# Kernel optimization log

Hardware: AMD Instinct MI355X
Metric: run time of the kernel (lower is better)

The kernel has to match this reference:

```python
import jax, jax.numpy as jnp
import numpy as np

B = 262144
NUM_FEA = 256          # input feature dim, split into two towers of 128
HIDDEN = [64, 32, 16]  # tower hidden units
CO_FEA = 32            # 2 * HIDDEN[-1], features entering co-attention
EMB = 8                # per-feature embedding dim
OUT_DIM = 16           # final Dense(16)


def setup_inputs() -> dict:
    key = jax.random.key(0)
    ks = jax.random.split(key, 12)
    mid = NUM_FEA // 2
    def glorot(k, shape):
        fan_in, fan_out = shape[0], shape[1]
        lim = np.sqrt(6.0 / (fan_in + fan_out)).astype(np.float32)
        return jax.random.uniform(k, shape, jnp.float32, -lim, lim)
    return {
        "x": jax.random.normal(ks[0], (B, NUM_FEA), jnp.float32),
        # shared tower (weight_share=True -> only mod_dnn1 is used)
        "W1": glorot(ks[1], (mid, HIDDEN[0])), "b1": jnp.zeros((HIDDEN[0],), jnp.float32),
        "W2": glorot(ks[2], (HIDDEN[0], HIDDEN[1])), "b2": jnp.zeros((HIDDEN[1],), jnp.float32),
        "W3": glorot(ks[3], (HIDDEN[1], HIDDEN[2])), "b3": jnp.zeros((HIDDEN[2],), jnp.float32),
        # 32 per-feature Dense(8) layers on scalar inputs, stacked: weight [32,8], bias [32,8]
        "W_emb": glorot(ks[4], (CO_FEA, EMB)),
        "b_emb": jnp.zeros((CO_FEA, EMB), jnp.float32),
        # bilinear co-attention matrix
        "M": glorot(ks[5], (EMB, EMB)),
        # final Dense(16, relu) for mix='concat'
        "W_out": glorot(ks[6], (CO_FEA, OUT_DIM)),
        "b_out": jnp.zeros((OUT_DIM,), jnp.float32),
    }


def reference(x, W1, b1, W2, b2, W3, b3, W_emb, b_emb, M, W_out, b_out):
    mid = x.shape[1] // 2

    def tower(h):
        h = jax.nn.relu(h @ W1 + b1)
        h = jax.nn.relu(h @ W2 + b2)
        h = jax.nn.relu(h @ W3 + b3)
        return h

    left = tower(x[:, :mid])      # [B,16]
    right = tower(x[:, mid:])     # [B,16] (weight_share=True)
    out = jnp.concatenate([left, right], axis=-1)  # [B,32]

    # 32 tiny Dense(emb) on scalar features, batched: [B,32,1]*[32,8] + [32,8]
    emb = out[:, :, None] * W_emb[None, :, :] + b_emb[None, :, :]  # [B,32,8]
    cmid = out.shape[1] // 2  # 16
    l, r = emb[:, :cmid, :], emb[:, cmid:, :]

    G = jnp.tanh(jnp.einsum('bie,ef,bjf->bij', l, M, r))  # [B,16,16]
    lr = jax.nn.softmax(G.sum(axis=1), axis=-1)           # [B,16]
    rl = jax.nn.softmax(G.sum(axis=2), axis=-1)           # [B,16]
    a = jnp.concatenate([lr, rl], axis=-1)                # [B,32]

    out = out * a
    # mix == 'concat' -> Dense(16, relu)
    return jax.nn.relu(out @ W_out + b_out)               # [B,16]
```

## Files before the change

### kernel.cpp

```cpp
#include <hip/hip_runtime.h>

typedef __attribute__((ext_vector_type(8))) short bf16x8;
typedef __attribute__((ext_vector_type(4))) float f32x4;

#define MFMA16(a, b, c) __builtin_amdgcn_mfma_f32_16x16x32_bf16(a, b, c, 0, 0, 0)

__device__ __forceinline__ unsigned short f2bf(float f) {
    unsigned u = __builtin_bit_cast(unsigned, f);
    u += 0x7FFFu + ((u >> 16) & 1u);
    return (unsigned short)(u >> 16);
}
__device__ __forceinline__ float bf2f(unsigned short h) {
    return __builtin_bit_cast(float, (unsigned)h << 16);
}

__device__ __forceinline__ void split8(const float* v, bf16x8& hi, bf16x8& lo) {
    unsigned* hp = reinterpret_cast<unsigned*>(&hi);
    unsigned* lp = reinterpret_cast<unsigned*>(&lo);
    #pragma unroll
    for (int q = 0; q < 4; ++q) {
        const float a = v[2 * q], b = v[2 * q + 1];
        unsigned hpair;
        asm("v_cvt_pk_bf16_f32 %0, %1, %2" : "=v"(hpair) : "v"(a), "v"(b));
        const float ha = __builtin_bit_cast(float, hpair << 16);
        const float hb = __builtin_bit_cast(float, hpair & 0xFFFF0000u);
        const float ra = a - ha, rb = b - hb;
        unsigned lpair;
        asm("v_cvt_pk_bf16_f32 %0, %1, %2" : "=v"(lpair) : "v"(ra), "v"(rb));
        hp[q] = hpair;
        lp[q] = lpair;
    }
}

__global__ void prep_kernel(const float* __restrict__ W1,
                            const float* __restrict__ W2,
                            const float* __restrict__ W3,
                            const float* __restrict__ W_emb,
                            const float* __restrict__ b_emb,
                            const float* __restrict__ M,
                            float* __restrict__ pqrs,
                            unsigned short* __restrict__ w1h,
                            unsigned short* __restrict__ w1l,
                            unsigned short* __restrict__ wsm) {
    const int t = threadIdx.x;
    const float C2 = 2.8853900817779268f;
    {
        const int j = t >> 4;
        const int i = t & 15;
        float mr[8], mb[8];
        #pragma unroll
        for (int e = 0; e < 8; ++e) {
            float ar = 0.f, ab = 0.f;
            #pragma unroll
            for (int f = 0; f < 8; ++f) {
                const float m = M[e * 8 + f];
                ar = fmaf(m, W_emb[(16 + j) * 8 + f], ar);
                ab = fmaf(m, b_emb[(16 + j) * 8 + f], ab);
            }
            mr[e] = ar; mb[e] = ab;
        }
        float P = 0.f, Q = 0.f, R = 0.f, S = 0.f;
        #pragma unroll
        for (int e = 0; e < 8; ++e) {
            const float lw = W_emb[i * 8 + e];
            const float lb = b_emb[i * 8 + e];
            P = fmaf(lw, mr[e], P);
            Q = fmaf(lw, mb[e], Q);
            R = fmaf(lb, mr[e], R);
            S = fmaf(lb, mb[e], S);
        }
        pqrs[0 * 256 + j * 16 + i] = C2 * P;
        pqrs[1 * 256 + j * 16 + i] = C2 * Q;
        pqrs[2 * 256 + j * 16 + i] = C2 * R;
        pqrs[3 * 256 + j * 16 + i] = C2 * S;
    }
    for (int e = 0; e < 32; ++e) {
        const int idx = t * 32 + e;
        const int i = idx & 7, lane = (idx >> 3) & 63;
        const int n = (idx >> 9) & 3, kt = idx >> 11;
        const int k = kt * 32 + (lane >> 4) * 8 + i;
        const int c = n * 16 + (lane & 15);
        const float v = W1[k * 64 + c];
        const unsigned short h = f2bf(v);
        w1h[idx] = h;
        w1l[idx] = f2bf(v - bf2f(h));
    }
    for (int e = 0; e < 8; ++e) {
        const int idx = t * 8 + e;
        const int i = idx & 7, lane = (idx >> 3) & 63;
        const int n = (idx >> 9) & 1, kt = (idx >> 10) & 1;
        const int k = kt * 32 + (lane >> 4) * 8 + i;
        const int c = n * 16 + (lane & 15);
        const float v = W2[k * 32 + c];
        const unsigned short h = f2bf(v);
        wsm[idx] = h;
        wsm[2048 + idx] = f2bf(v - bf2f(h));
    }
    for (int e = 0; e < 2; ++e) {
        const int idx = t * 2 + e;
        const int i = idx & 7, lane = (idx >> 3) & 63;
        const int k = (lane >> 4) * 8 + i;
        const int c = lane & 15;
        const float v = W3[k * 16 + c];
        const unsigned short h = f2bf(v);
        wsm[4096 + idx] = h;
        wsm[4608 + idx] = f2bf(v - bf2f(h));
    }
}

__global__ __launch_bounds__(256, 3) void fused_kernel(
    const float* __restrict__ x,
    const unsigned short* __restrict__ w1h,
    const unsigned short* __restrict__ w1l,
    const unsigned short* __restrict__ wsm,
    const float* __restrict__ b1, const float* __restrict__ b2,
    const float* __restrict__ b3,
    const float* __restrict__ pqrs,
    const float* __restrict__ W_out, const float* __restrict__ b_out,
    float* __restrict__ y) {
    __shared__ float s_tr[4][16 * 68];
    __shared__ float s_h3[4][16 * 130];

    const int tid = threadIdx.x;
    const int l  = tid & 63;
    const int wv = tid >> 6;
    const int lm = l & 15;
    const int lg = l >> 4;

    const unsigned short* w2h = wsm;
    const unsigned short* w2l = wsm + 2048;
    const unsigned short* w3h = wsm + 4096;
    const unsigned short* w3l = wsm + 4608;

    float b1v[4], b2v[2];
    #pragma unroll
    for (int n = 0; n < 4; ++n) b1v[n] = b1[n * 16 + lm];
    #pragma unroll
    for (int n = 0; n < 2; ++n) b2v[n] = b2[n * 16 + lm];
    const float b3v = b3[lm];

    const long tr0 = (long)blockIdx.x * 512 + wv * 128;
    float* tb  = s_tr[wv];
    float* h3b = s_h3[wv];

    float4 xb[2][8];
    {
        const float* xp = x + (tr0 + lm) * 128 + lg * 8;
        #pragma unroll
        for (int kt = 0; kt < 4; ++kt) {
            xb[0][2 * kt]     = *(const float4*)(xp + kt * 32);
            xb[0][2 * kt + 1] = *(const float4*)(xp + kt * 32 + 4);
        }
    }

    #pragma unroll
    for (int tile = 0; tile < 8; ++tile) {
        const int cur = tile & 1, nxt = cur ^ 1;
        if (tile < 7) {
            const float* xp = x + (tr0 + (tile + 1) * 16 + lm) * 128 + lg * 8;
            #pragma unroll
            for (int kt = 0; kt < 4; ++kt) {
                xb[nxt][2 * kt]     = *(const float4*)(xp + kt * 32);
                xb[nxt][2 * kt + 1] = *(const float4*)(xp + kt * 32 + 4);
            }
        }
        f32x4 acc[4];
        #pragma unroll
        for (int n = 0; n < 4; ++n) acc[n] = f32x4{b1v[n], b1v[n], b1v[n], b1v[n]};
        #pragma unroll
        for (int kt = 0; kt < 4; ++kt) {
            const float4 a = xb[cur][2 * kt], b = xb[cur][2 * kt + 1];
            const float xv[8] = {a.x, a.y, a.z, a.w, b.x, b.y, b.z, b.w};
            bf16x8 xh, xl; split8(xv, xh, xl);
            #pragma unroll
            for (int n = 0; n < 4; ++n) {
                const int fo = ((kt * 4 + n) * 64 + l) * 8;
                const bf16x8 wh = *(const bf16x8*)(w1h + fo);
                const bf16x8 wl = *(const bf16x8*)(w1l + fo);
                acc[n] = MFMA16(xh, wh, acc[n]);
                acc[n] = MFMA16(xl, wh, acc[n]);
                acc[n] = MFMA16(xh, wl, acc[n]);
            }
        }
        #pragma unroll
        for (int n = 0; n < 4; ++n)
            #pragma unroll
            for (int r = 0; r < 4; ++r)
                tb[(lg * 4 + r) * 68 + n * 16 + lm] = fmaxf(acc[n][r], 0.f);
        f32x4 acc2[2];
        #pragma unroll
        for (int n = 0; n < 2; ++n) acc2[n] = f32x4{b2v[n], b2v[n], b2v[n], b2v[n]};
        #pragma unroll
        for (int kt = 0; kt < 2; ++kt) {
            const float* ap = tb + lm * 68 + kt * 32 + lg * 8;
            const float4 h0 = *(const float4*)(ap);
            const float4 h1 = *(const float4*)(ap + 4);
            const float hv[8] = {h0.x, h0.y, h0.z, h0.w, h1.x, h1.y, h1.z, h1.w};
            bf16x8 hh, hl; split8(hv, hh, hl);
            #pragma unroll
            for (int n = 0; n < 2; ++n) {
                const int fo = ((kt * 2 + n) * 64 + l) * 8;
                const bf16x8 wh = *(const bf16x8*)(w2h + fo);
                const bf16x8 wl = *(const bf16x8*)(w2l + fo);
                acc2[n] = MFMA16(hh, wh, acc2[n]);
                acc2[n] = MFMA16(hl, wh, acc2[n]);
                acc2[n] = MFMA16(hh, wl, acc2[n]);
            }
        }
        #pragma unroll
        for (int n = 0; n < 2; ++n)
            #pragma unroll
            for (int r = 0; r < 4; ++r)
                tb[(lg * 4 + r) * 68 + n * 16 + lm] = fmaxf(acc2[n][r], 0.f);
        f32x4 acc3 = f32x4{b3v, b3v, b3v, b3v};
        {
            const float* ap = tb + lm * 68 + lg * 8;
            const float4 h0 = *(const float4*)(ap);
            const float4 h1 = *(const float4*)(ap + 4);
            const float hv[8] = {h0.x, h0.y, h0.z, h0.w, h1.x, h1.y, h1.z, h1.w};
            bf16x8 hh, hl; split8(hv, hh, hl);
            const bf16x8 wh = *(const bf16x8*)(w3h + l * 8);
            const bf16x8 wl = *(const bf16x8*)(w3l + l * 8);
            acc3 = MFMA16(hh, wh, acc3);
            acc3 = MFMA16(hl, wh, acc3);
            acc3 = MFMA16(hh, wl, acc3);
        }
        #pragma unroll
        for (int r = 0; r < 4; ++r)
            h3b[lm * 130 + tile * 16 + lg * 4 + r] = fmaxf(acc3[r], 0.f);
    }

    float oL[16], oR[16];
    #pragma unroll
    for (int c = 0; c < 16; ++c) {
        const float2 v = *(const float2*)(h3b + c * 130 + 2 * l);
        oL[c] = v.x;
        oR[c] = v.y;
    }

    float sir[16];
    #pragma unroll
    for (int i = 0; i < 16; ++i) sir[i] = 0.f;
    float sjv[16];
    #pragma unroll
    for (int j = 0; j < 16; ++j) {
        const float r = oR[j];
        const float* __restrict__ Pr = pqrs +       j * 16;
        const float* __restrict__ Qr = pqrs + 256 + j * 16;
        const float* __restrict__ Rr = pqrs + 512 + j * 16;
        const float* __restrict__ Sr = pqrs + 768 + j * 16;
        float accr = 0.f;
        #pragma unroll
        for (int i = 0; i < 16; ++i) {
            const float t1 = fmaf(r, Pr[i], Qr[i]);
            const float t2 = fmaf(r, Rr[i], Sr[i]);
            const float z  = fmaf(oL[i], t1, t2);
            const float e  = __builtin_amdgcn_exp2f(z);
            const float rc = __builtin_amdgcn_rcpf(e + 1.0f);
            accr   += rc;
            sir[i] += rc;
        }
        sjv[j] = accr;
    }
    #pragma unroll
    for (int i = 0; i < 16; ++i) {
        sjv[i] = fmaf(-2.f, sjv[i], 16.f);
        sir[i] = fmaf(-2.f, sir[i], 16.f);
    }

    {
        float mx = sjv[0];
        #pragma unroll
        for (int i = 1; i < 16; ++i) mx = fmaxf(mx, sjv[i]);
        float s = 0.f; float ex[16];
        #pragma unroll
        for (int i = 0; i < 16; ++i) { ex[i] = __expf(sjv[i] - mx); s += ex[i]; }
        const float inv = __builtin_amdgcn_rcpf(s);
        #pragma unroll
        for (int i = 0; i < 16; ++i) oL[i] *= ex[i] * inv;
    }
    {
        float mx = sir[0];
        #pragma unroll
        for (int i = 1; i < 16; ++i) mx = fmaxf(mx, sir[i]);
        float s = 0.f; float ex[16];
        #pragma unroll
        for (int i = 0; i < 16; ++i) { ex[i] = __expf(sir[i] - mx); s += ex[i]; }
        const float inv = __builtin_amdgcn_rcpf(s);
        #pragma unroll
        for (int i = 0; i < 16; ++i) oR[i] *= ex[i] * inv;
    }

    float yv[16];
    #pragma unroll
    for (int oo = 0; oo < 16; ++oo) yv[oo] = b_out[oo];
    #pragma unroll
    for (int c = 0; c < 16; ++c) {
        const float cl = oL[c];
        const float cr = oR[c];
        const float* __restrict__ wl = W_out + c * 16;
        const float* __restrict__ wt = W_out + (16 + c) * 16;
        #pragma unroll
        for (int oo = 0; oo < 16; ++oo) {
            yv[oo] = fmaf(cl, wl[oo], yv[oo]);
            yv[oo] = fmaf(cr, wt[oo], yv[oo]);
        }
    }

    float* __restrict__ yo = y + ((tr0 >> 1) + l) * 16;
    #pragma unroll
    for (int q = 0; q < 4; ++q) {
        float4 v;
        v.x = fmaxf(yv[q * 4 + 0], 0.f);
        v.y = fmaxf(yv[q * 4 + 1], 0.f);
        v.z = fmaxf(yv[q * 4 + 2], 0.f);
        v.w = fmaxf(yv[q * 4 + 3], 0.f);
        *reinterpret_cast<float4*>(yo + q * 4) = v;
    }
}

extern "C" void kernel_launch(void* const* d_in, const int* in_sizes, int n_in,
                              void* d_out, int out_size, void* d_ws, size_t ws_size,
                              hipStream_t stream) {
    const float* x     = (const float*)d_in[0];
    const float* W1    = (const float*)d_in[1];
    const float* b1    = (const float*)d_in[2];
    const float* W2    = (const float*)d_in[3];
    const float* b2    = (const float*)d_in[4];
    const float* W3    = (const float*)d_in[5];
    const float* b3    = (const float*)d_in[6];
    const float* W_emb = (const float*)d_in[7];
    const float* b_emb = (const float*)d_in[8];
    const float* M     = (const float*)d_in[9];
    const float* W_out = (const float*)d_in[10];
    const float* b_out = (const float*)d_in[11];
    float* y = (float*)d_out;

    float* pqrs = (float*)d_ws;
    unsigned short* w1h = (unsigned short*)((char*)d_ws + 4096);
    unsigned short* w1l = w1h + 8192;
    unsigned short* wsm = w1l + 8192;

    const int nrows = in_sizes[0] / 256;

    prep_kernel<<<1, 256, 0, stream>>>(W1, W2, W3, W_emb, b_emb, M,
                                       pqrs, w1h, w1l, wsm);
    const int grid = nrows / 256;
    fused_kernel<<<grid, 256, 0, stream>>>(x, w1h, w1l, wsm,
                                           b1, b2, b3, pqrs, W_out, b_out, y);
}
```

Baseline: 132.2 us.

## Halve rows per wave and split each batch row across lane pairs

Each wave now processes 64 tower rows (32 batch rows) instead of 128, and the grid doubles. The h3 staging buffer is transposed so each lane reads its own 16-wide tower output as four float4 loads. Paired lanes exchange halves with __shfl_xor so both hold the left and right features, and each writes half of the 16-wide output. The co-attention and output layers now run redundantly on both lanes of a pair. This trades doubled tail arithmetic for more parallelism, a shorter per-wave loop and simpler LDS access.

```diff
diff --git a/kernel.cpp b/kernel.cpp
--- a/kernel.cpp
+++ b/kernel.cpp
@@ -119,7 +119,7 @@
     const float* __restrict__ W_out, const float* __restrict__ b_out,
     float* __restrict__ y) {
     __shared__ float s_tr[4][16 * 68];
-    __shared__ float s_h3[4][16 * 130];
+    __shared__ float s_h3[4][64 * 20];
 
     const int tid = threadIdx.x;
     const int l  = tid & 63;
@@ -139,7 +139,7 @@
     for (int n = 0; n < 2; ++n) b2v[n] = b2[n * 16 + lm];
     const float b3v = b3[lm];
 
-    const long tr0 = (long)blockIdx.x * 512 + wv * 128;
+    const long tr0 = (long)blockIdx.x * 256 + wv * 64;
     float* tb  = s_tr[wv];
     float* h3b = s_h3[wv];
 
@@ -154,9 +154,9 @@
     }
 
     #pragma unroll
-    for (int tile = 0; tile < 8; ++tile) {
+    for (int tile = 0; tile < 4; ++tile) {
         const int cur = tile & 1, nxt = cur ^ 1;
-        if (tile < 7) {
+        if (tile < 3) {
             const float* xp = x + (tr0 + (tile + 1) * 16 + lm) * 128 + lg * 8;
             #pragma unroll
             for (int kt = 0; kt < 4; ++kt) {
@@ -227,15 +227,25 @@
         }
         #pragma unroll
         for (int r = 0; r < 4; ++r)
-            h3b[lm * 130 + tile * 16 + lg * 4 + r] = fmaxf(acc3[r], 0.f);
-    }
-
+            h3b[(tile * 16 + lg * 4 + r) * 20 + lm] = fmaxf(acc3[r], 0.f);
+    }
+
+    const int p = l & 1;
+    float o[16];
+    {
+        const float4* hp = (const float4*)(h3b + l * 20);
+        const float4 t0 = hp[0], t1 = hp[1], t2 = hp[2], t3 = hp[3];
+        o[0] = t0.x;  o[1] = t0.y;  o[2] = t0.z;  o[3] = t0.w;
+        o[4] = t1.x;  o[5] = t1.y;  o[6] = t1.z;  o[7] = t1.w;
+        o[8] = t2.x;  o[9] = t2.y;  o[10] = t2.z; o[11] = t2.w;
+        o[12] = t3.x; o[13] = t3.y; o[14] = t3.z; o[15] = t3.w;
+    }
     float oL[16], oR[16];
     #pragma unroll
-    for (int c = 0; c < 16; ++c) {
-        const float2 v = *(const float2*)(h3b + c * 130 + 2 * l);
-        oL[c] = v.x;
-        oR[c] = v.y;
+    for (int i = 0; i < 16; ++i) {
+        const float oth = __shfl_xor(o[i], 1);
+        oL[i] = p ? oth : o[i];
+        oR[i] = p ? o[i] : oth;
     }
 
     float sir[16];
@@ -306,17 +316,17 @@
             yv[oo] = fmaf(cr, wt[oo], yv[oo]);
         }
     }
-
-    float* __restrict__ yo = y + ((tr0 >> 1) + l) * 16;
-    #pragma unroll
-    for (int q = 0; q < 4; ++q) {
-        float4 v;
-        v.x = fmaxf(yv[q * 4 + 0], 0.f);
-        v.y = fmaxf(yv[q * 4 + 1], 0.f);
-        v.z = fmaxf(yv[q * 4 + 2], 0.f);
-        v.w = fmaxf(yv[q * 4 + 3], 0.f);
-        *reinterpret_cast<float4*>(yo + q * 4) = v;
-    }
+    #pragma unroll
+    for (int oo = 0; oo < 16; ++oo) yv[oo] = fmaxf(yv[oo], 0.f);
+
+    float4 v0, v1;
+    v0.x = p ? yv[8]  : yv[0]; v0.y = p ? yv[9]  : yv[1];
+    v0.z = p ? yv[10] : yv[2]; v0.w = p ? yv[11] : yv[3];
+    v1.x = p ? yv[12] : yv[4]; v1.y = p ? yv[13] : yv[5];
+    v1.z = p ? yv[14] : yv[6]; v1.w = p ? yv[15] : yv[7];
+    float* __restrict__ yo = y + ((tr0 >> 1) + (l >> 1)) * 16 + p * 8;
+    *reinterpret_cast<float4*>(yo)     = v0;
+    *reinterpret_cast<float4*>(yo + 4) = v1;
 }
 
 extern "C" void kernel_launch(void* const* d_in, const int* in_sizes, int n_in,
@@ -345,7 +355,7 @@
 
     prep_kernel<<<1, 256, 0, stream>>>(W1, W2, W3, W_emb, b_emb, M,
                                        pqrs, w1h, w1l, wsm);
-    const int grid = nrows / 256;
+    const int grid = nrows / 128;
     fused_kernel<<<grid, 256, 0, stream>>>(x, w1h, w1l, wsm,
                                            b1, b2, b3, pqrs, W_out, b_out, y);
 }
```

After: 141.4 us. 1.07x slower.
